# Performance work log

Hardware: AMD Instinct MI355X
Metric: run time of the kernel (lower is better)

The kernel has to match this reference:

```python
import jax, jax.numpy as jnp
import numpy as np

_OFF = [(dz, dy, dx) for dz in (-1, 0, 1) for dy in (-1, 0, 1) for dx in (-1, 0, 1)]
_K3 = [(kz, ky, kx) for kz in range(3) for ky in range(3) for kx in range(3)]


def _key(c, dims):
    D, H, W = dims
    return ((c[:, 0].astype(np.int64) * D + c[:, 1]) * H + c[:, 2]) * W + c[:, 3]


def _dedupe(c, dims):
    k = _key(c, dims)
    _, idx = np.unique(k, return_index=True)
    return c[np.sort(idx)]


def _make_lookup(coords, dims):
    D, H, W = dims
    keys = _key(coords, dims)
    order = np.argsort(keys)
    skeys = keys[order]

    def query(qc):
        valid = ((qc[:, 1] >= 0) & (qc[:, 1] < D) & (qc[:, 2] >= 0) & (qc[:, 2] < H)
                 & (qc[:, 3] >= 0) & (qc[:, 3] < W))
        qk = _key(np.where(valid[:, None], qc, 0), dims)
        pos = np.clip(np.searchsorted(skeys, qk), 0, len(skeys) - 1)
        hit = valid & (skeys[pos] == qk)
        return np.where(hit, order[pos], -1).astype(np.int32)
    return query


def _subm_nbr(coords, query):
    nbr = np.empty((len(coords), 27), np.int32)
    for ki, (dz, dy, dx) in enumerate(_OFF):
        qc = coords.copy()
        qc[:, 1] += dz; qc[:, 2] += dy; qc[:, 3] += dx
        nbr[:, ki] = query(qc)
    return nbr


def _down(in_coords, pads, out_dims, in_query):
    # spconv SparseConv3d k=3 s=2: output active set + gather rulebook (in = 2*out - p + k)
    p = np.array(pads)
    cand = []
    for k in _K3:
        t = in_coords[:, 1:] + p - np.array(k)
        m = (t % 2 == 0).all(1)
        o = t[m] // 2
        ok = (o >= 0).all(1) & (o < np.array(out_dims)).all(1)
        cand.append(np.concatenate([in_coords[m][ok][:, :1], o[ok]], 1))
    out_coords = _dedupe(np.concatenate(cand), out_dims)
    nbrd = np.empty((len(out_coords), 27), np.int32)
    for ki, k in enumerate(_K3):
        qc = out_coords.copy()
        qc[:, 1:] = out_coords[:, 1:] * 2 - p + np.array(k)
        nbrd[:, ki] = in_query(qc)
    return out_coords, nbrd


def _inv(in_coords, pads, out_query):
    # inverse conv: for each stride-s input voxel i, gather downsampled voxel o = (i+p-k)/2
    p = np.array(pads)
    nbr = np.full((len(in_coords), 27), -1, np.int32)
    for ki, k in enumerate(_K3):
        t = in_coords[:, 1:] + p - np.array(k)
        div = (t % 2 == 0).all(1)
        qc = in_coords.copy()
        qc[:, 1:] = np.where(div[:, None], t // 2, -1)
        nbr[:, ki] = np.where(div, out_query(qc), -1)
    return nbr


def setup_inputs() -> dict:
    rng = np.random.default_rng(0)
    B, K, P, STD = 4, 160, 128, 3.0
    D1 = (41, 1024, 1024)  # sparse_shape (z, y, x)
    pts = []
    for b in range(B):
        ctr = np.stack([rng.uniform(2, d - 3, K) for d in D1], 1)
        pb = ctr[:, None, :] + rng.normal(0.0, STD, (K, P, 3))
        pb = np.clip(np.rint(pb.reshape(-1, 3)), 0, np.array(D1) - 1).astype(np.int64)
        pts.append(np.concatenate([np.full((len(pb), 1), b, np.int64), pb], 1))
    c1 = _dedupe(np.concatenate(pts), D1)
    D2 = tuple((d + 2 * q - 3) // 2 + 1 for d, q in zip(D1, (1, 1, 1)))
    D3 = tuple((d + 2 * q - 3) // 2 + 1 for d, q in zip(D2, (1, 1, 1)))
    D4 = tuple((d + 2 * q - 3) // 2 + 1 for d, q in zip(D3, (0, 1, 1)))
    q1 = _make_lookup(c1, D1); nbr1 = _subm_nbr(c1, q1)
    c2, nbrd2 = _down(c1, (1, 1, 1), D2, q1); q2 = _make_lookup(c2, D2); nbr2 = _subm_nbr(c2, q2)
    c3, nbrd3 = _down(c2, (1, 1, 1), D3, q2); q3 = _make_lookup(c3, D3); nbr3 = _subm_nbr(c3, q3)
    c4, nbrd4 = _down(c3, (0, 1, 1), D4, q3); q4 = _make_lookup(c4, D4); nbr4 = _subm_nbr(c4, q4)
    nbri4 = _inv(c3, (0, 1, 1), q4)
    nbri3 = _inv(c2, (1, 1, 1), q3)
    nbri2 = _inv(c1, (1, 1, 1), q2)
    N1 = len(c1)
    w = lambda *s: jnp.asarray((0.05 * rng.standard_normal(s)).astype(np.float32))
    bn = lambda n, c: jnp.asarray(np.stack([1.0 + 0.02 * rng.standard_normal((n, c)),
                                            0.02 * rng.standard_normal((n, c))], 1).astype(np.float32))
    return {
        'voxel_feat': jnp.asarray(rng.standard_normal((N1, 4)).astype(np.float32)),
        'Win': w(27, 4, 32),
        'W32': w(10, 27, 32, 32),
        'W64': w(10, 27, 64, 64),
        'Wd3': w(27, 32, 64),
        'W6432': w(3, 27, 64, 32),
        'W12864': w(2, 27, 128, 64),
        'bn32': bn(14, 32),
        'bn64': bn(13, 64),
        'nbr1': jnp.asarray(nbr1), 'nbr2': jnp.asarray(nbr2),
        'nbr3': jnp.asarray(nbr3), 'nbr4': jnp.asarray(nbr4),
        'nbrd2': jnp.asarray(nbrd2), 'nbrd3': jnp.asarray(nbrd3), 'nbrd4': jnp.asarray(nbrd4),
        'nbri4': jnp.asarray(nbri4), 'nbri3': jnp.asarray(nbri3), 'nbri2': jnp.asarray(nbri2),
    }


def _conv(feat, nbr, W):
    # rulebook gather-matmul-scatter: out[n] = sum_k feat[nbr[n,k]] @ W[k]
    out = jnp.zeros((nbr.shape[0], W.shape[-1]), feat.dtype)
    for k in range(27):
        idx = nbr[:, k]
        g = jnp.where((idx >= 0)[:, None], feat[jnp.maximum(idx, 0)], 0.0)
        out = out + g @ W[k]
    return out


def _block(f, nbr, W, sb):  # conv + (folded, eval-mode) BN + ReLU
    return jax.nn.relu(_conv(f, nbr, W) * sb[0] + sb[1])


def _basic(f, nbr, Wa, sa, Wb, sb):  # SparseBasicBlock
    h = jax.nn.relu(_conv(f, nbr, Wa) * sa[0] + sa[1])
    h = _conv(h, nbr, Wb) * sb[0] + sb[1]
    return jax.nn.relu(h + f)


def _reduce(c, oc):  # channel_reduction: view(n, oc, -1).sum(2)
    return c.reshape(c.shape[0], oc, -1).sum(-1)


def _forward(voxel_feat, Win, W32, W64, Wd3, W6432, W12864, bn32, bn64,
             nbr1, nbr2, nbr3, nbr4, nbrd2, nbrd3, nbrd4, nbri4, nbri3, nbri2):
    x = _block(voxel_feat, nbr1, Win, bn32[0])       # conv_input
    x1 = _block(x, nbr1, W32[0], bn32[1])            # conv1
    h = _block(x1, nbrd2, W32[1], bn32[2])           # spconv2 stride-2
    h = _block(h, nbr2, W32[2], bn32[3])
    x2 = _block(h, nbr2, W32[3], bn32[4])
    h = _block(x2, nbrd3, Wd3, bn64[0])              # spconv3 stride-2, 32->64
    h = _block(h, nbr3, W64[0], bn64[1])
    x3 = _block(h, nbr3, W64[1], bn64[2])
    h = _block(x3, nbrd4, W64[2], bn64[3])           # spconv4 stride-2, pad (0,1,1)
    h = _block(h, nbr4, W64[3], bn64[4])
    x4 = _block(h, nbr4, W64[4], bn64[5])
    # UR block 4 (lateral = bottom = x4)
    t = _basic(x4, nbr4, W64[5], bn64[6], W64[6], bn64[7])
    cat = jnp.concatenate([x4, t], 1)                # [N4, 128]
    x = _block(cat, nbr4, W12864[0], bn64[11]) + _reduce(cat, 64)
    xu4 = _block(x, nbri4, W64[7], bn64[8])          # inverseconv -> level 3
    # UR block 3
    t = _basic(x3, nbr3, W64[8], bn64[9], W64[9], bn64[10])
    cat = jnp.concatenate([xu4, t], 1)
    x = _block(cat, nbr3, W12864[1], bn64[12]) + _reduce(cat, 64)
    xu3 = _block(x, nbri3, W6432[0], bn32[11])       # inverseconv -> level 2, 32ch
    # UR block 2
    t = _basic(x2, nbr2, W32[4], bn32[5], W32[5], bn32[6])
    cat = jnp.concatenate([xu3, t], 1)
    x = _block(cat, nbr2, W6432[1], bn32[12]) + _reduce(cat, 32)
    xu2 = _block(x, nbri2, W32[6], bn32[7])          # inverseconv -> level 1
    # UR block 1 (conv_inv = conv5, submanifold at level 1)
    t = _basic(x1, nbr1, W32[7], bn32[8], W32[8], bn32[9])
    cat = jnp.concatenate([xu2, t], 1)
    x = _block(cat, nbr1, W6432[2], bn32[13]) + _reduce(cat, 32)
    return _block(x, nbr1, W32[9], bn32[10])         # conv5 -> unet_voxel_feat [N1, 32]


def reference(voxel_feat, Win, W32, W64, Wd3, W6432, W12864, bn32, bn64,
              nbr1, nbr2, nbr3, nbr4, nbrd2, nbrd3, nbrd4, nbri4, nbri3, nbri2):
    return _forward(voxel_feat, Win, W32, W64, Wd3, W6432, W12864, bn32, bn64,
                    nbr1, nbr2, nbr3, nbr4, nbrd2, nbrd3, nbrd4, nbri4, nbri3, nbri2)
```

## Files before the change

### kernel.cpp

```cpp
#include <hip/hip_runtime.h>


template<int CIN_A, int CIN_B, int COUT, int EPI>
__global__ __launch_bounds__(256) void spconv(
    const float* __restrict__ inA,
    const float* __restrict__ inB,
    const int*   __restrict__ nbr,
    const float* __restrict__ W,
    const float* __restrict__ bn,
    const float* __restrict__ skip,
    float*       __restrict__ out,
    int N)
{
    constexpr int CIN   = CIN_A + CIN_B;
    constexpr int COL_T = COUT / 4;
    constexpr int ROW_T = 256 / COL_T;
    constexpr int BM    = ROW_T * 4;
    constexpr int V     = CIN / 4;

    __shared__ int   s_nbr[BM * 27];
    __shared__ float s_G[CIN][BM];
    __shared__ float s_W[CIN * COUT];

    const int tid  = threadIdx.x;
    const int tx   = tid % COL_T;
    const int ty   = tid / COL_T;
    const int row0 = blockIdx.x * BM;

    for (int e = tid; e < BM * 27; e += 256) {
        int r = row0 + e / 27;
        s_nbr[e] = (r < N) ? nbr[(size_t)row0 * 27 + e] : -1;
    }

    float acc[4][4];
    #pragma unroll
    for (int i = 0; i < 4; ++i)
        #pragma unroll
        for (int j = 0; j < 4; ++j) acc[i][j] = 0.f;

    for (int k = 0; k < 27; ++k) {
        __syncthreads();
        constexpr int WQ = CIN * COUT / 4;
        const float4* Wg = reinterpret_cast<const float4*>(W + (size_t)k * CIN * COUT);
        #pragma unroll 1
        for (int e = tid; e < WQ; e += 256)
            reinterpret_cast<float4*>(s_W)[e] = Wg[e];
        #pragma unroll 1
        for (int e = tid; e < BM * V; e += 256) {
            int r  = e % BM;
            int c4 = e / BM;
            int idx = s_nbr[r * 27 + k];
            float4 v = make_float4(0.f, 0.f, 0.f, 0.f);
            if (idx >= 0) {
                if (CIN_B == 0 || c4 * 4 < CIN_A)
                    v = *reinterpret_cast<const float4*>(inA + (size_t)idx * CIN_A + c4 * 4);
                else
                    v = *reinterpret_cast<const float4*>(inB + (size_t)idx * CIN_B + c4 * 4 - CIN_A);
            }
            s_G[c4 * 4 + 0][r] = v.x;
            s_G[c4 * 4 + 1][r] = v.y;
            s_G[c4 * 4 + 2][r] = v.z;
            s_G[c4 * 4 + 3][r] = v.w;
        }
        __syncthreads();
        #pragma unroll 16
        for (int ci = 0; ci < CIN; ++ci) {
            float4 g = *reinterpret_cast<const float4*>(&s_G[ci][ty * 4]);
            float4 w = *reinterpret_cast<const float4*>(&s_W[ci * COUT + tx * 4]);
            acc[0][0] += g.x * w.x; acc[0][1] += g.x * w.y; acc[0][2] += g.x * w.z; acc[0][3] += g.x * w.w;
            acc[1][0] += g.y * w.x; acc[1][1] += g.y * w.y; acc[1][2] += g.y * w.z; acc[1][3] += g.y * w.w;
            acc[2][0] += g.z * w.x; acc[2][1] += g.z * w.y; acc[2][2] += g.z * w.z; acc[2][3] += g.z * w.w;
            acc[3][0] += g.w * w.x; acc[3][1] += g.w * w.y; acc[3][2] += g.w * w.z; acc[3][3] += g.w * w.w;
        }
    }

    const int co0 = tx * 4;
    float4 sc = *reinterpret_cast<const float4*>(bn + co0);
    float4 bi = *reinterpret_cast<const float4*>(bn + COUT + co0);
    #pragma unroll
    for (int i = 0; i < 4; ++i) {
        int r = row0 + ty * 4 + i;
        if (r >= N) break;
        float4 y;
        y.x = acc[i][0] * sc.x + bi.x;
        y.y = acc[i][1] * sc.y + bi.y;
        y.z = acc[i][2] * sc.z + bi.z;
        y.w = acc[i][3] * sc.w + bi.w;
        if (EPI == 1) {
            float4 s = *reinterpret_cast<const float4*>(skip + (size_t)r * COUT + co0);
            y.x += s.x; y.y += s.y; y.z += s.z; y.w += s.w;
        }
        y.x = fmaxf(y.x, 0.f); y.y = fmaxf(y.y, 0.f);
        y.z = fmaxf(y.z, 0.f); y.w = fmaxf(y.w, 0.f);
        if (EPI == 2) {
            const float* rs = (2 * co0 < CIN_A)
                ? inA + (size_t)r * CIN_A + 2 * co0
                : inB + (size_t)r * CIN_B + 2 * co0 - CIN_A;
            float4 p0 = reinterpret_cast<const float4*>(rs)[0];
            float4 p1 = reinterpret_cast<const float4*>(rs)[1];
            y.x += p0.x + p0.y; y.y += p0.z + p0.w;
            y.z += p1.x + p1.y; y.w += p1.z + p1.w;
        }
        *reinterpret_cast<float4*>(out + (size_t)r * COUT + co0) = y;
    }
}

extern "C" void kernel_launch(void* const* d_in, const int* in_sizes, int n_in,
                              void* d_out, int out_size, void* d_ws, size_t ws_size,
                              hipStream_t stream)
{
    (void)n_in; (void)out_size; (void)ws_size;
    const float* vf     = (const float*)d_in[0];
    const float* Win    = (const float*)d_in[1];
    const float* W32    = (const float*)d_in[2];
    const float* W64    = (const float*)d_in[3];
    const float* Wd3    = (const float*)d_in[4];
    const float* W6432  = (const float*)d_in[5];
    const float* W12864 = (const float*)d_in[6];
    const float* bn32   = (const float*)d_in[7];
    const float* bn64   = (const float*)d_in[8];
    const int* nbr1  = (const int*)d_in[9];
    const int* nbr2  = (const int*)d_in[10];
    const int* nbr3  = (const int*)d_in[11];
    const int* nbr4  = (const int*)d_in[12];
    const int* nbrd2 = (const int*)d_in[13];
    const int* nbrd3 = (const int*)d_in[14];
    const int* nbrd4 = (const int*)d_in[15];
    const int* nbri4 = (const int*)d_in[16];
    const int* nbri3 = (const int*)d_in[17];
    const int* nbri2 = (const int*)d_in[18];

    const int N1 = in_sizes[9]  / 27;
    const int N2 = in_sizes[10] / 27;
    const int N3 = in_sizes[11] / 27;
    const int N4 = in_sizes[12] / 27;

    float* ws = (float*)d_ws;
    size_t off = 0;
    auto alloc = [&](size_t n) { float* p = ws + off; off += n; return p; };
    float* X1  = alloc((size_t)N1 * 32);
    float* TA  = alloc((size_t)N1 * 32);
    float* TA2 = alloc((size_t)N1 * 32);
    float* TU1 = alloc((size_t)N1 * 32);
    float* X2  = alloc((size_t)N2 * 32);
    float* TB2 = alloc((size_t)N2 * 32);
    float* TC2 = alloc((size_t)N2 * 32);
    float* TU2 = alloc((size_t)N2 * 32);
    float* X3  = alloc((size_t)N3 * 64);
    float* TB3 = alloc((size_t)N3 * 64);
    float* TC3 = alloc((size_t)N3 * 64);
    float* TU3 = alloc((size_t)N3 * 64);
    float* X4  = alloc((size_t)N4 * 64);
    float* TB4 = alloc((size_t)N4 * 64);
    float* TC4 = alloc((size_t)N4 * 64);
    float* OUT = (float*)d_out;

    auto G32 = [](int N){ return dim3((unsigned)((N + 127) / 128)); };
    auto G64 = [](int N){ return dim3((unsigned)((N + 63) / 64)); };

    const size_t S32 = 27*32*32, S64 = (size_t)27*64*64, S6432 = (size_t)27*64*32, S12864 = (size_t)27*128*64;

    spconv<4,0,32,0><<<G32(N1),256,0,stream>>>(vf, nullptr, nbr1, Win, bn32+0*64, nullptr, TA, N1);
    spconv<32,0,32,0><<<G32(N1),256,0,stream>>>(TA, nullptr, nbr1, W32+0*S32, bn32+1*64, nullptr, X1, N1);
    spconv<32,0,32,0><<<G32(N2),256,0,stream>>>(X1, nullptr, nbrd2, W32+1*S32, bn32+2*64, nullptr, TB2, N2);
    spconv<32,0,32,0><<<G32(N2),256,0,stream>>>(TB2, nullptr, nbr2, W32+2*S32, bn32+3*64, nullptr, TC2, N2);
    spconv<32,0,32,0><<<G32(N2),256,0,stream>>>(TC2, nullptr, nbr2, W32+3*S32, bn32+4*64, nullptr, X2, N2);
    spconv<32,0,64,0><<<G64(N3),256,0,stream>>>(X2, nullptr, nbrd3, Wd3, bn64+0*128, nullptr, TB3, N3);
    spconv<64,0,64,0><<<G64(N3),256,0,stream>>>(TB3, nullptr, nbr3, W64+0*S64, bn64+1*128, nullptr, TC3, N3);
    spconv<64,0,64,0><<<G64(N3),256,0,stream>>>(TC3, nullptr, nbr3, W64+1*S64, bn64+2*128, nullptr, X3, N3);
    spconv<64,0,64,0><<<G64(N4),256,0,stream>>>(X3, nullptr, nbrd4, W64+2*S64, bn64+3*128, nullptr, TB4, N4);
    spconv<64,0,64,0><<<G64(N4),256,0,stream>>>(TB4, nullptr, nbr4, W64+3*S64, bn64+4*128, nullptr, TC4, N4);
    spconv<64,0,64,0><<<G64(N4),256,0,stream>>>(TC4, nullptr, nbr4, W64+4*S64, bn64+5*128, nullptr, X4, N4);
    spconv<64,0,64,0><<<G64(N4),256,0,stream>>>(X4, nullptr, nbr4, W64+5*S64, bn64+6*128, nullptr, TB4, N4);
    spconv<64,0,64,1><<<G64(N4),256,0,stream>>>(TB4, nullptr, nbr4, W64+6*S64, bn64+7*128, X4, TC4, N4);
    spconv<64,64,64,2><<<G64(N4),256,0,stream>>>(X4, TC4, nbr4, W12864+0*S12864, bn64+11*128, nullptr, TB4, N4);
    spconv<64,0,64,0><<<G64(N3),256,0,stream>>>(TB4, nullptr, nbri4, W64+7*S64, bn64+8*128, nullptr, TU3, N3);
    spconv<64,0,64,0><<<G64(N3),256,0,stream>>>(X3, nullptr, nbr3, W64+8*S64, bn64+9*128, nullptr, TB3, N3);
    spconv<64,0,64,1><<<G64(N3),256,0,stream>>>(TB3, nullptr, nbr3, W64+9*S64, bn64+10*128, X3, TC3, N3);
    spconv<64,64,64,2><<<G64(N3),256,0,stream>>>(TU3, TC3, nbr3, W12864+1*S12864, bn64+12*128, nullptr, TB3, N3);
    spconv<64,0,32,0><<<G32(N2),256,0,stream>>>(TB3, nullptr, nbri3, W6432+0*S6432, bn32+11*64, nullptr, TU2, N2);
    spconv<32,0,32,0><<<G32(N2),256,0,stream>>>(X2, nullptr, nbr2, W32+4*S32, bn32+5*64, nullptr, TB2, N2);
    spconv<32,0,32,1><<<G32(N2),256,0,stream>>>(TB2, nullptr, nbr2, W32+5*S32, bn32+6*64, X2, TC2, N2);
    spconv<32,32,32,2><<<G32(N2),256,0,stream>>>(TU2, TC2, nbr2, W6432+1*S6432, bn32+12*64, nullptr, TB2, N2);
    spconv<32,0,32,0><<<G32(N1),256,0,stream>>>(TB2, nullptr, nbri2, W32+6*S32, bn32+7*64, nullptr, TU1, N1);
    spconv<32,0,32,0><<<G32(N1),256,0,stream>>>(X1, nullptr, nbr1, W32+7*S32, bn32+8*64, nullptr, TA, N1);
    spconv<32,0,32,1><<<G32(N1),256,0,stream>>>(TA, nullptr, nbr1, W32+8*S32, bn32+9*64, X1, TA2, N1);
    spconv<32,32,32,2><<<G32(N1),256,0,stream>>>(TU1, TA2, nbr1, W6432+2*S6432, bn32+13*64, nullptr, TA, N1);
    spconv<32,0,32,0><<<G32(N1),256,0,stream>>>(TA, nullptr, nbr1, W32+9*S32, bn32+10*64, nullptr, OUT, N1);
}
```

Baseline: 4.384 ms.

## Split kernel taps across workgroups for small levels, prefetch next tap into registers

Adds a split-K path for small layers: the 27 kernel taps are divided among 3 or 9 workgroups per row block, which write partial sums to a workspace buffer, and a separate epilogue kernel reduces them and applies BN, skip and residual. Independently, the main loop now loads the next tap's gathered features and weights into registers while the current tap computes, overlapping global loads with FMA work. Workgroup IDs are also remapped so consecutive logical blocks land on the same XCD. This targets GPU under-utilisation on the deep, low-voxel-count levels, at the cost of extra partial-sum traffic, one more launch per split conv, and higher register pressure.

New measurement: 4.098 ms. 1.07x faster.

```diff
diff --git a/kernel.cpp b/kernel.cpp
--- a/kernel.cpp
+++ b/kernel.cpp
@@ -1,7 +1,7 @@
 #include <hip/hip_runtime.h>
 
 
-template<int CIN_A, int CIN_B, int COUT, int EPI>
+template<int CIN_A, int CIN_B, int COUT, int EPI, bool SPLIT>
 __global__ __launch_bounds__(256) void spconv(
     const float* __restrict__ inA,
     const float* __restrict__ inB,
@@ -10,63 +10,112 @@
     const float* __restrict__ bn,
     const float* __restrict__ skip,
     float*       __restrict__ out,
-    int N)
+    float*       __restrict__ pout,
+    int N, int KS)
 {
     constexpr int CIN   = CIN_A + CIN_B;
+    constexpr int BM    = (COUT == 32) ? 128 : 64;
     constexpr int COL_T = COUT / 4;
     constexpr int ROW_T = 256 / COL_T;
-    constexpr int BM    = ROW_T * 4;
+    static_assert(ROW_T * 4 == BM, "tile mismatch");
     constexpr int V     = CIN / 4;
+    constexpr int GTOT  = BM * V;
+    constexpr int GPT   = (GTOT + 255) / 256;
+    constexpr int CSTR  = 256 / BM;
+    constexpr int WTOT  = CIN * COUT / 4;
+    constexpr int WPT   = (WTOT + 255) / 256;
 
     __shared__ int   s_nbr[BM * 27];
     __shared__ float s_G[CIN][BM];
     __shared__ float s_W[CIN * COUT];
 
-    const int tid  = threadIdx.x;
-    const int tx   = tid % COL_T;
-    const int ty   = tid / COL_T;
-    const int row0 = blockIdx.x * BM;
+    const int tid = threadIdx.x;
+    const int tx  = tid % COL_T;
+    const int ty  = tid / COL_T;
+
+    unsigned nwg = gridDim.x;
+    unsigned q8 = nwg / 8u, r8 = nwg % 8u;
+    unsigned xcd = blockIdx.x % 8u, sub = blockIdx.x / 8u;
+    unsigned id = (xcd < r8 ? xcd * (q8 + 1u) : r8 * (q8 + 1u) + (xcd - r8) * q8) + sub;
+
+    int rb, k0, k1, kg;
+    if (SPLIT) {
+        kg = (int)(id % (unsigned)KS);
+        rb = (int)(id / (unsigned)KS);
+        int kper = 27 / KS;
+        k0 = kg * kper; k1 = k0 + kper;
+    } else {
+        kg = 0; rb = (int)id; k0 = 0; k1 = 27;
+    }
+    const int row0 = rb * BM;
 
     for (int e = tid; e < BM * 27; e += 256) {
-        int r = row0 + e / 27;
-        s_nbr[e] = (r < N) ? nbr[(size_t)row0 * 27 + e] : -1;
-    }
-
-    float acc[4][4];
-    #pragma unroll
-    for (int i = 0; i < 4; ++i)
-        #pragma unroll
-        for (int j = 0; j < 4; ++j) acc[i][j] = 0.f;
-
-    for (int k = 0; k < 27; ++k) {
+        int rr = row0 + e / 27;
+        s_nbr[e] = (rr < N) ? nbr[(size_t)row0 * 27 + e] : -1;
+    }
+    __syncthreads();
+
+    const int gr  = tid % BM;
+    const int gc0 = tid / BM;
+    float4 gv[GPT];
+    float4 wv[WPT];
+
+    auto load_tap = [&](int k) {
+        int idx = s_nbr[gr * 27 + k];
+        #pragma unroll
+        for (int j = 0; j < GPT; ++j) {
+            int e = tid + j * 256;
+            if ((GTOT % 256 == 0) || e < GTOT) {
+                int c4 = gc0 + j * CSTR;
+                float4 v = make_float4(0.f, 0.f, 0.f, 0.f);
+                if (idx >= 0) {
+                    if (CIN_B == 0 || c4 * 4 < CIN_A)
+                        v = *(const float4*)(inA + (size_t)idx * CIN_A + c4 * 4);
+                    else
+                        v = *(const float4*)(inB + (size_t)idx * CIN_B + c4 * 4 - CIN_A);
+                }
+                gv[j] = v;
+            }
+        }
+        const float4* Wg = (const float4*)(W + (size_t)k * CIN * COUT);
+        #pragma unroll
+        for (int j = 0; j < WPT; ++j) {
+            int e = tid + j * 256;
+            if ((WTOT % 256 == 0) || e < WTOT) wv[j] = Wg[e];
+        }
+    };
+
+    auto store_tap = [&]() {
+        #pragma unroll
+        for (int j = 0; j < GPT; ++j) {
+            int e = tid + j * 256;
+            if ((GTOT % 256 == 0) || e < GTOT) {
+                int c4 = gc0 + j * CSTR;
+                s_G[c4 * 4 + 0][gr] = gv[j].x;
+                s_G[c4 * 4 + 1][gr] = gv[j].y;
+                s_G[c4 * 4 + 2][gr] = gv[j].z;
+                s_G[c4 * 4 + 3][gr] = gv[j].w;
+            }
+        }
+        #pragma unroll
+        for (int j = 0; j < WPT; ++j) {
+            int e = tid + j * 256;
+            if ((WTOT % 256 == 0) || e < WTOT) ((float4*)s_W)[e] = wv[j];
+        }
+    };
+
+    float acc[4][4] = {};
+    load_tap(k0);
+
+    for (int k = k0; k < k1; ++k) {
         __syncthreads();
-        constexpr int WQ = CIN * COUT / 4;
-        const float4* Wg = reinterpret_cast<const float4*>(W + (size_t)k * CIN * COUT);
-        #pragma unroll 1
-        for (int e = tid; e < WQ; e += 256)
-            reinterpret_cast<float4*>(s_W)[e] = Wg[e];
-        #pragma unroll 1
-        for (int e = tid; e < BM * V; e += 256) {
-            int r  = e % BM;
-            int c4 = e / BM;
-            int idx = s_nbr[r * 27 + k];
-            float4 v = make_float4(0.f, 0.f, 0.f, 0.f);
-            if (idx >= 0) {
-                if (CIN_B == 0 || c4 * 4 < CIN_A)
-                    v = *reinterpret_cast<const float4*>(inA + (size_t)idx * CIN_A + c4 * 4);
-                else
-                    v = *reinterpret_cast<const float4*>(inB + (size_t)idx * CIN_B + c4 * 4 - CIN_A);
-            }
-            s_G[c4 * 4 + 0][r] = v.x;
-            s_G[c4 * 4 + 1][r] = v.y;
-            s_G[c4 * 4 + 2][r] = v.z;
-            s_G[c4 * 4 + 3][r] = v.w;
-        }
+        store_tap();
         __syncthreads();
+        if (k + 1 < k1) load_tap(k + 1);
         #pragma unroll 16
         for (int ci = 0; ci < CIN; ++ci) {
-            float4 g = *reinterpret_cast<const float4*>(&s_G[ci][ty * 4]);
-            float4 w = *reinterpret_cast<const float4*>(&s_W[ci * COUT + tx * 4]);
+            float4 g = *(const float4*)&s_G[ci][ty * 4];
+            float4 w = *(const float4*)&s_W[ci * COUT + tx * 4];
             acc[0][0] += g.x * w.x; acc[0][1] += g.x * w.y; acc[0][2] += g.x * w.z; acc[0][3] += g.x * w.w;
             acc[1][0] += g.y * w.x; acc[1][1] += g.y * w.y; acc[1][2] += g.y * w.z; acc[1][3] += g.y * w.w;
             acc[2][0] += g.z * w.x; acc[2][1] += g.z * w.y; acc[2][2] += g.z * w.z; acc[2][3] += g.z * w.w;
@@ -75,34 +124,91 @@
     }
 
     const int co0 = tx * 4;
-    float4 sc = *reinterpret_cast<const float4*>(bn + co0);
-    float4 bi = *reinterpret_cast<const float4*>(bn + COUT + co0);
-    #pragma unroll
-    for (int i = 0; i < 4; ++i) {
-        int r = row0 + ty * 4 + i;
-        if (r >= N) break;
-        float4 y;
-        y.x = acc[i][0] * sc.x + bi.x;
-        y.y = acc[i][1] * sc.y + bi.y;
-        y.z = acc[i][2] * sc.z + bi.z;
-        y.w = acc[i][3] * sc.w + bi.w;
-        if (EPI == 1) {
-            float4 s = *reinterpret_cast<const float4*>(skip + (size_t)r * COUT + co0);
-            y.x += s.x; y.y += s.y; y.z += s.z; y.w += s.w;
-        }
-        y.x = fmaxf(y.x, 0.f); y.y = fmaxf(y.y, 0.f);
-        y.z = fmaxf(y.z, 0.f); y.w = fmaxf(y.w, 0.f);
-        if (EPI == 2) {
-            const float* rs = (2 * co0 < CIN_A)
-                ? inA + (size_t)r * CIN_A + 2 * co0
-                : inB + (size_t)r * CIN_B + 2 * co0 - CIN_A;
-            float4 p0 = reinterpret_cast<const float4*>(rs)[0];
-            float4 p1 = reinterpret_cast<const float4*>(rs)[1];
-            y.x += p0.x + p0.y; y.y += p0.z + p0.w;
-            y.z += p1.x + p1.y; y.w += p1.z + p1.w;
-        }
-        *reinterpret_cast<float4*>(out + (size_t)r * COUT + co0) = y;
-    }
+    if (SPLIT) {
+        #pragma unroll
+        for (int i = 0; i < 4; ++i) {
+            int rr = row0 + ty * 4 + i;
+            if (rr < N) {
+                float4 y = make_float4(acc[i][0], acc[i][1], acc[i][2], acc[i][3]);
+                *(float4*)(pout + ((size_t)kg * N + rr) * COUT + co0) = y;
+            }
+        }
+    } else {
+        float4 sc = *(const float4*)(bn + co0);
+        float4 bi = *(const float4*)(bn + COUT + co0);
+        #pragma unroll
+        for (int i = 0; i < 4; ++i) {
+            int rr = row0 + ty * 4 + i;
+            if (rr >= N) break;
+            float4 y;
+            y.x = acc[i][0] * sc.x + bi.x;
+            y.y = acc[i][1] * sc.y + bi.y;
+            y.z = acc[i][2] * sc.z + bi.z;
+            y.w = acc[i][3] * sc.w + bi.w;
+            if (EPI == 1) {
+                float4 s = *(const float4*)(skip + (size_t)rr * COUT + co0);
+                y.x += s.x; y.y += s.y; y.z += s.z; y.w += s.w;
+            }
+            y.x = fmaxf(y.x, 0.f); y.y = fmaxf(y.y, 0.f);
+            y.z = fmaxf(y.z, 0.f); y.w = fmaxf(y.w, 0.f);
+            if (EPI == 2) {
+                const float* rs = (2 * co0 < CIN_A)
+                    ? inA + (size_t)rr * CIN_A + 2 * co0
+                    : inB + (size_t)rr * CIN_B + 2 * co0 - CIN_A;
+                float4 p0 = ((const float4*)rs)[0];
+                float4 p1 = ((const float4*)rs)[1];
+                y.x += p0.x + p0.y; y.y += p0.z + p0.w;
+                y.z += p1.x + p1.y; y.w += p1.z + p1.w;
+            }
+            *(float4*)(out + (size_t)rr * COUT + co0) = y;
+        }
+    }
+}
+
+template<int CIN_A, int CIN_B, int COUT, int EPI>
+__global__ __launch_bounds__(256) void epi_k(
+    const float* __restrict__ P, int KS,
+    const float* __restrict__ bn,
+    const float* __restrict__ skip,
+    const float* __restrict__ inA,
+    const float* __restrict__ inB,
+    float* __restrict__ out, int N)
+{
+    int t = blockIdx.x * 256 + threadIdx.x;
+    int total = N * (COUT / 4);
+    if (t >= total) return;
+    int r   = t / (COUT / 4);
+    int co0 = (t % (COUT / 4)) * 4;
+
+    float4 y = make_float4(0.f, 0.f, 0.f, 0.f);
+    for (int kg = 0; kg < KS; ++kg) {
+        float4 p = *(const float4*)(P + ((size_t)kg * N + r) * COUT + co0);
+        y.x += p.x; y.y += p.y; y.z += p.z; y.w += p.w;
+    }
+    float4 sc = *(const float4*)(bn + co0);
+    float4 bi = *(const float4*)(bn + COUT + co0);
+    y.x = y.x * sc.x + bi.x; y.y = y.y * sc.y + bi.y;
+    y.z = y.z * sc.z + bi.z; y.w = y.w * sc.w + bi.w;
+    if (EPI == 1) {
+        float4 s = *(const float4*)(skip + (size_t)r * COUT + co0);
+        y.x += s.x; y.y += s.y; y.z += s.z; y.w += s.w;
+    }
+    y.x = fmaxf(y.x, 0.f); y.y = fmaxf(y.y, 0.f);
+    y.z = fmaxf(y.z, 0.f); y.w = fmaxf(y.w, 0.f);
+    if (EPI == 2) {
+        const float* rs = (2 * co0 < CIN_A)
+            ? inA + (size_t)r * CIN_A + 2 * co0
+            : inB + (size_t)r * CIN_B + 2 * co0 - CIN_A;
+        float4 p0 = ((const float4*)rs)[0];
+        float4 p1 = ((const float4*)rs)[1];
+        y.x += p0.x + p0.y; y.y += p0.z + p0.w;
+        y.z += p1.x + p1.y; y.w += p1.z + p1.w;
+    }
+    *(float4*)(out + (size_t)r * COUT + co0) = y;
+}
+
+static inline int ksel(int nblk) {
+    return nblk >= 512 ? 1 : (nblk >= 170 ? 3 : 9);
 }
 
 extern "C" void kernel_launch(void* const* d_in, const int* in_sizes, int n_in,
@@ -155,36 +261,62 @@
     float* TC4 = alloc((size_t)N4 * 64);
     float* OUT = (float*)d_out;
 
-    auto G32 = [](int N){ return dim3((unsigned)((N + 127) / 128)); };
-    auto G64 = [](int N){ return dim3((unsigned)((N + 63) / 64)); };
+    auto pneed = [&](int N, int BM, int CO) -> size_t {
+        int nb = (N + BM - 1) / BM; int ks = ksel(nb);
+        return ks > 1 ? (size_t)ks * N * CO : 0;
+    };
+    size_t maxP = 0;
+    size_t c;
+    c = pneed(N1, 128, 32); if (c > maxP) maxP = c;
+    c = pneed(N2, 128, 32); if (c > maxP) maxP = c;
+    c = pneed(N3,  64, 64); if (c > maxP) maxP = c;
+    c = pneed(N4,  64, 64); if (c > maxP) maxP = c;
+    float* P = alloc(maxP);
 
     const size_t S32 = 27*32*32, S64 = (size_t)27*64*64, S6432 = (size_t)27*64*32, S12864 = (size_t)27*128*64;
 
-    spconv<4,0,32,0><<<G32(N1),256,0,stream>>>(vf, nullptr, nbr1, Win, bn32+0*64, nullptr, TA, N1);
-    spconv<32,0,32,0><<<G32(N1),256,0,stream>>>(TA, nullptr, nbr1, W32+0*S32, bn32+1*64, nullptr, X1, N1);
-    spconv<32,0,32,0><<<G32(N2),256,0,stream>>>(X1, nullptr, nbrd2, W32+1*S32, bn32+2*64, nullptr, TB2, N2);
-    spconv<32,0,32,0><<<G32(N2),256,0,stream>>>(TB2, nullptr, nbr2, W32+2*S32, bn32+3*64, nullptr, TC2, N2);
-    spconv<32,0,32,0><<<G32(N2),256,0,stream>>>(TC2, nullptr, nbr2, W32+3*S32, bn32+4*64, nullptr, X2, N2);
-    spconv<32,0,64,0><<<G64(N3),256,0,stream>>>(X2, nullptr, nbrd3, Wd3, bn64+0*128, nullptr, TB3, N3);
-    spconv<64,0,64,0><<<G64(N3),256,0,stream>>>(TB3, nullptr, nbr3, W64+0*S64, bn64+1*128, nullptr, TC3, N3);
-    spconv<64,0,64,0><<<G64(N3),256,0,stream>>>(TC3, nullptr, nbr3, W64+1*S64, bn64+2*128, nullptr, X3, N3);
-    spconv<64,0,64,0><<<G64(N4),256,0,stream>>>(X3, nullptr, nbrd4, W64+2*S64, bn64+3*128, nullptr, TB4, N4);
-    spconv<64,0,64,0><<<G64(N4),256,0,stream>>>(TB4, nullptr, nbr4, W64+3*S64, bn64+4*128, nullptr, TC4, N4);
-    spconv<64,0,64,0><<<G64(N4),256,0,stream>>>(TC4, nullptr, nbr4, W64+4*S64, bn64+5*128, nullptr, X4, N4);
-    spconv<64,0,64,0><<<G64(N4),256,0,stream>>>(X4, nullptr, nbr4, W64+5*S64, bn64+6*128, nullptr, TB4, N4);
-    spconv<64,0,64,1><<<G64(N4),256,0,stream>>>(TB4, nullptr, nbr4, W64+6*S64, bn64+7*128, X4, TC4, N4);
-    spconv<64,64,64,2><<<G64(N4),256,0,stream>>>(X4, TC4, nbr4, W12864+0*S12864, bn64+11*128, nullptr, TB4, N4);
-    spconv<64,0,64,0><<<G64(N3),256,0,stream>>>(TB4, nullptr, nbri4, W64+7*S64, bn64+8*128, nullptr, TU3, N3);
-    spconv<64,0,64,0><<<G64(N3),256,0,stream>>>(X3, nullptr, nbr3, W64+8*S64, bn64+9*128, nullptr, TB3, N3);
-    spconv<64,0,64,1><<<G64(N3),256,0,stream>>>(TB3, nullptr, nbr3, W64+9*S64, bn64+10*128, X3, TC3, N3);
-    spconv<64,64,64,2><<<G64(N3),256,0,stream>>>(TU3, TC3, nbr3, W12864+1*S12864, bn64+12*128, nullptr, TB3, N3);
-    spconv<64,0,32,0><<<G32(N2),256,0,stream>>>(TB3, nullptr, nbri3, W6432+0*S6432, bn32+11*64, nullptr, TU2, N2);
-    spconv<32,0,32,0><<<G32(N2),256,0,stream>>>(X2, nullptr, nbr2, W32+4*S32, bn32+5*64, nullptr, TB2, N2);
-    spconv<32,0,32,1><<<G32(N2),256,0,stream>>>(TB2, nullptr, nbr2, W32+5*S32, bn32+6*64, X2, TC2, N2);
-    spconv<32,32,32,2><<<G32(N2),256,0,stream>>>(TU2, TC2, nbr2, W6432+1*S6432, bn32+12*64, nullptr, TB2, N2);
-    spconv<32,0,32,0><<<G32(N1),256,0,stream>>>(TB2, nullptr, nbri2, W32+6*S32, bn32+7*64, nullptr, TU1, N1);
-    spconv<32,0,32,0><<<G32(N1),256,0,stream>>>(X1, nullptr, nbr1, W32+7*S32, bn32+8*64, nullptr, TA, N1);
-    spconv<32,0,32,1><<<G32(N1),256,0,stream>>>(TA, nullptr, nbr1, W32+8*S32, bn32+9*64, X1, TA2, N1);
-    spconv<32,32,32,2><<<G32(N1),256,0,stream>>>(TU1, TA2, nbr1, W6432+2*S6432, bn32+13*64, nullptr, TA, N1);
-    spconv<32,0,32,0><<<G32(N1),256,0,stream>>>(TA, nullptr, nbr1, W32+9*S32, bn32+10*64, nullptr, OUT, N1);
+#define CONV(CA, CB, CO, EP, pA, pB, pN, pW, pBN, pS, pO, NN) do {                      \
+        constexpr int BM_ = ((CO) == 32) ? 128 : 64;                                    \
+        int nblk_ = ((NN) + BM_ - 1) / BM_;                                             \
+        int ks_ = ksel(nblk_);                                                          \
+        if (ks_ == 1) {                                                                 \
+            spconv<CA, CB, CO, EP, false><<<dim3((unsigned)nblk_), 256, 0, stream>>>(   \
+                pA, pB, pN, pW, pBN, pS, pO, nullptr, NN, 1);                           \
+        } else {                                                                        \
+            spconv<CA, CB, CO, EP, true><<<dim3((unsigned)(nblk_ * ks_)), 256, 0, stream>>>( \
+                pA, pB, pN, pW, pBN, pS, nullptr, P, NN, ks_);                          \
+            int tot4_ = (NN) * ((CO) / 4);                                              \
+            epi_k<CA, CB, CO, EP><<<dim3((unsigned)((tot4_ + 255) / 256)), 256, 0, stream>>>( \
+                P, ks_, pBN, pS, pA, pB, pO, NN);                                       \
+        }                                                                               \
+    } while (0)
+
+    CONV(4,0,32,0,  vf,  nullptr, nbr1,  Win,         bn32+0*64,  nullptr, TA,  N1);
+    CONV(32,0,32,0, TA,  nullptr, nbr1,  W32+0*S32,   bn32+1*64,  nullptr, X1,  N1);
+    CONV(32,0,32,0, X1,  nullptr, nbrd2, W32+1*S32,   bn32+2*64,  nullptr, TB2, N2);
+    CONV(32,0,32,0, TB2, nullptr, nbr2,  W32+2*S32,   bn32+3*64,  nullptr, TC2, N2);
+    CONV(32,0,32,0, TC2, nullptr, nbr2,  W32+3*S32,   bn32+4*64,  nullptr, X2,  N2);
+    CONV(32,0,64,0, X2,  nullptr, nbrd3, Wd3,         bn64+0*128, nullptr, TB3, N3);
+    CONV(64,0,64,0, TB3, nullptr, nbr3,  W64+0*S64,   bn64+1*128, nullptr, TC3, N3);
+    CONV(64,0,64,0, TC3, nullptr, nbr3,  W64+1*S64,   bn64+2*128, nullptr, X3,  N3);
+    CONV(64,0,64,0, X3,  nullptr, nbrd4, W64+2*S64,   bn64+3*128, nullptr, TB4, N4);
+    CONV(64,0,64,0, TB4, nullptr, nbr4,  W64+3*S64,   bn64+4*128, nullptr, TC4, N4);
+    CONV(64,0,64,0, TC4, nullptr, nbr4,  W64+4*S64,   bn64+5*128, nullptr, X4,  N4);
+    CONV(64,0,64,0, X4,  nullptr, nbr4,  W64+5*S64,   bn64+6*128, nullptr, TB4, N4);
+    CONV(64,0,64,1, TB4, nullptr, nbr4,  W64+6*S64,   bn64+7*128, X4,      TC4, N4);
+    CONV(64,64,64,2, X4, TC4,     nbr4,  W12864+0*S12864, bn64+11*128, nullptr, TB4, N4);
+    CONV(64,0,64,0, TB4, nullptr, nbri4, W64+7*S64,   bn64+8*128, nullptr, TU3, N3);
+    CONV(64,0,64,0, X3,  nullptr, nbr3,  W64+8*S64,   bn64+9*128, nullptr, TB3, N3);
+    CONV(64,0,64,1, TB3, nullptr, nbr3,  W64+9*S64,   bn64+10*128, X3,     TC3, N3);
+    CONV(64,64,64,2, TU3, TC3,    nbr3,  W12864+1*S12864, bn64+12*128, nullptr, TB3, N3);
+    CONV(64,0,32,0, TB3, nullptr, nbri3, W6432+0*S6432, bn32+11*64, nullptr, TU2, N2);
+    CONV(32,0,32,0, X2,  nullptr, nbr2,  W32+4*S32,   bn32+5*64,  nullptr, TB2, N2);
+    CONV(32,0,32,1, TB2, nullptr, nbr2,  W32+5*S32,   bn32+6*64,  X2,      TC2, N2);
+    CONV(32,32,32,2, TU2, TC2,    nbr2,  W6432+1*S6432, bn32+12*64, nullptr, TB2, N2);
+    CONV(32,0,32,0, TB2, nullptr, nbri2, W32+6*S32,   bn32+7*64,  nullptr, TU1, N1);
+    CONV(32,0,32,0, X1,  nullptr, nbr1,  W32+7*S32,   bn32+8*64,  nullptr, TA,  N1);
+    CONV(32,0,32,1, TA,  nullptr, nbr1,  W32+8*S32,   bn32+9*64,  X1,      TA2, N1);
+    CONV(32,32,32,2, TU1, TA2,    nbr1,  W6432+2*S6432, bn32+13*64, nullptr, TA,  N1);
+    CONV(32,0,32,0, TA,  nullptr, nbr1,  W32+9*S32,   bn32+10*64, nullptr, OUT, N1);
+#undef CONV
 }
```
